# Kernel tuning notes

Hardware: AMD Instinct MI355X
Metric: run time of the kernel (lower is better)

The kernel has to match this reference:

```python
import jax, jax.numpy as jnp
import numpy as np

K = 3
KK = K * K


def _offset_mask_conv(x, ow, ob):
    # Conv2d(C_in, 3*KK, k=3, stride=1, pad=1) in NCHW/OIHW
    y = jax.lax.conv_general_dilated(
        x, ow, window_strides=(1, 1), padding=((1, 1), (1, 1)),
        dimension_numbers=('NCHW', 'OIHW', 'NCHW'))
    return y + ob[None, :, None, None]


def _bilinear(xb, gy, gx):
    # xb: [C,H,W]; gy,gx: [KK,H,W] pixel coords (align_corners=True => pixel==unnormalized)
    # padding_mode='zeros': out-of-range taps contribute 0.
    C, H, W = xb.shape
    x0f = jnp.floor(gx); y0f = jnp.floor(gy)
    x0 = x0f.astype(jnp.int32); y0 = y0f.astype(jnp.int32)
    x1 = x0 + 1; y1 = y0 + 1
    wx1 = gx - x0f; wy1 = gy - y0f
    wx0 = 1.0 - wx1; wy0 = 1.0 - wy1

    def gather(yi, xi):
        valid = (yi >= 0) & (yi < H) & (xi >= 0) & (xi < W)
        yc = jnp.clip(yi, 0, H - 1)
        xc = jnp.clip(xi, 0, W - 1)
        v = xb[:, yc, xc]  # [C,KK,H,W]
        return v * valid[None].astype(xb.dtype)

    return (gather(y0, x0) * (wy0 * wx0)[None]
            + gather(y0, x1) * (wy0 * wx1)[None]
            + gather(y1, x0) * (wy1 * wx0)[None]
            + gather(y1, x1) * (wy1 * wx1)[None])  # [C,KK,H,W]


def setup_inputs() -> dict:
    key = jax.random.key(0)
    k1, k2, k3, k4 = jax.random.split(key, 4)
    B, C, Cout, H, W = 8, 64, 64, 128, 128
    x = jax.random.normal(k1, (B, C, H, W), dtype=jnp.float32)
    # offset/mask conv params (small, so offsets stay in a realistic range)
    ow = jax.random.normal(k2, (3 * KK, C, K, K), dtype=jnp.float32) * 0.01
    ob = jnp.zeros((3 * KK,), dtype=jnp.float32)
    # main conv weight (kaiming-ish scale) and bias
    w = jax.random.normal(k3, (Cout, C, K, K), dtype=jnp.float32) * (1.0 / np.sqrt(C * KK))
    b = jax.random.normal(k4, (Cout,), dtype=jnp.float32) * 0.01
    return {"x": x, "ow": ow, "ob": ob, "w": w, "b": b}


def reference(x, ow, ob, w, b):
    B, C, H, W = x.shape
    om = _offset_mask_conv(x, ow, ob)            # [B, 3*KK, H, W]
    off_x = om[:, :KK]                           # o1 -> x-offset
    off_y = om[:, KK:2 * KK]                     # o2 -> y-offset
    mask = jax.nn.sigmoid(om[:, 2 * KK:])        # [B,KK,H,W]

    gh, gw = jnp.meshgrid(jnp.arange(H, dtype=x.dtype), jnp.arange(W, dtype=x.dtype), indexing='ij')
    d = jnp.arange(-(K // 2), K // 2 + 1, dtype=x.dtype)
    kh, kw = jnp.meshgrid(d, d, indexing='ij')
    dh = kh.reshape(-1)                          # [KK] row-major (dh,dw) order matches weight[...,i,j]
    dw = kw.reshape(-1)

    gx = gw[None, None] + dw[None, :, None, None] + off_x   # [B,KK,H,W]
    gy = gh[None, None] + dh[None, :, None, None] + off_y

    sampled = jax.vmap(_bilinear)(x, gy, gx)     # [B,C,KK,H,W]
    sampled = sampled * mask[:, None]            # modulation

    wflat = w.reshape(w.shape[0], w.shape[1], KK)  # [Cout,C,KK]
    out = jnp.einsum('bckhw,ock->bohw', sampled, wflat) + b[None, :, None, None]
    return out
```

## Files before the change

### kernel.cpp

```cpp
#include <hip/hip_runtime.h>

#define B 8
#define C 64
#define H 128
#define W 128
#define HW (H * W)
#define OC 27
#define KK 9
#define COUT 64
#define KDIM 576
#define LDSROW 1152
#define NPIX 32
#define NMETA (NPIX * KK)

typedef __attribute__((ext_vector_type(8))) short s16x8;
typedef __attribute__((ext_vector_type(4))) float f32x4;

__device__ inline ushort f2bf(float f) {
    union { float f; unsigned u; } uv;
    uv.f = f;
    unsigned r = uv.u + 0x7FFF + ((uv.u >> 16) & 1);
    return (ushort)(r >> 16);
}
__device__ inline float bf2f(ushort u) {
    return __uint_as_float((unsigned)u << 16);
}

__global__ __launch_bounds__(256) void k_transpose_x(const float* __restrict__ x,
                                                     ushort* __restrict__ xTb) {
    __shared__ float lds[64][65];
    int j = blockIdx.x;
    int vb = (j & 7) * 256 + (j >> 3);
    int b = vb >> 8;
    int tile = vb & 255;
    int hw0 = tile * 64;
    int lane = threadIdx.x & 63;
    int cg = threadIdx.x >> 6;
#pragma unroll
    for (int r = 0; r < 16; ++r) {
        int c = cg * 16 + r;
        lds[c][lane] = x[(size_t)(b * C + c) * HW + hw0 + lane];
    }
    __syncthreads();
#pragma unroll
    for (int r = 0; r < 16; ++r) {
        int hwl = cg * 16 + r;
        xTb[(size_t)(b * HW + hw0 + hwl) * C + lane] = f2bf(lds[lane][hwl]);
    }
}

__global__ __launch_bounds__(256) void k_prep_w(const float* __restrict__ w,
                                                ushort* __restrict__ wB) {
    int idx = blockIdx.x * 256 + threadIdx.x;
    if (idx >= COUT * KDIM) return;
    int o = idx / KDIM;
    int Kx = idx % KDIM;
    int k = Kx >> 6;
    int c = Kx & 63;
    wB[idx] = f2bf(w[(size_t)(o * C + c) * KK + k]);
}

__global__ __launch_bounds__(256) void k_prep_aw(const float* __restrict__ ow,
                                                 ushort* __restrict__ awB) {
    int idx = blockIdx.x * 256 + threadIdx.x;
    if (idx >= 32 * KDIM) return;
    int o = idx / KDIM;
    int Kx = idx % KDIM;
    int tap = Kx >> 6;
    int c = Kx & 63;
    float v = (o < OC) ? ow[((size_t)o * C + c) * KK + tap] : 0.0f;
    awB[idx] = f2bf(v);
}

__global__ __launch_bounds__(256) void k_om(const ushort* __restrict__ xTb,
                                            const ushort* __restrict__ awB,
                                            const float* __restrict__ ob,
                                            float* __restrict__ om_pm) {
    __shared__ __align__(16) char xwin[3 * 66 * 128];
    int tid = threadIdx.x;
    int lane = tid & 63;
    int wv = tid >> 6;
    int j = blockIdx.x;
    int vb = (j & 7) * 256 + (j >> 3);
    int b = vb >> 8;
    int h = (vb >> 1) & 127;
    int w0 = (vb & 1) * 64;

    const ushort* xb = xTb + (size_t)b * (HW * C);
    int ch2 = tid & 31;
#pragma unroll
    for (int it = 0; it < 25; ++it) {
        int pi = it * 8 + (tid >> 5);
        if (pi < 198) {
            int row = pi / 66;
            int col = pi - row * 66;
            int y = h - 1 + row;
            int xc = w0 - 1 + col;
            unsigned v = 0;
            if ((unsigned)y < H && (unsigned)xc < W)
                v = *(const unsigned*)(xb + ((size_t)(y * W + xc) << 6) + ch2 * 2);
            int byte = (pi * 128 + ch2 * 4) ^ ((col & 7) << 4);
            *(unsigned*)(xwin + byte) = v;
        }
    }
    __syncthreads();

    f32x4 acc0 = {0.f, 0.f, 0.f, 0.f};
    f32x4 acc1 = {0.f, 0.f, 0.f, 0.f};
    int pixl = lane & 15;
    int q = lane >> 4;
    int base_col = wv * 16 + pixl;
    const ushort* a0 = awB + (size_t)pixl * KDIM + q * 8;
    const ushort* a1 = awB + (size_t)(16 + pixl) * KDIM + q * 8;
#pragma unroll
    for (int s = 0; s < 18; ++s) {
        int tap = s >> 1;
        int row = tap / 3;
        int cs = tap - row * 3;
        int col = base_col + cs;
        int c0b = ((s & 1) * 32 + q * 8) * 2;
        int byte = (((row * 66 + col) << 7) + c0b) ^ ((col & 7) << 4);
        s16x8 bfrag = *(const s16x8*)(xwin + byte);
        s16x8 af0 = *(const s16x8*)(a0 + s * 32);
        s16x8 af1 = *(const s16x8*)(a1 + s * 32);
        acc0 = __builtin_amdgcn_mfma_f32_16x16x32_bf16(af0, bfrag, acc0, 0, 0, 0);
        acc1 = __builtin_amdgcn_mfma_f32_16x16x32_bf16(af1, bfrag, acc1, 0, 0, 0);
    }

    __syncthreads();
    float* omt = (float*)xwin;
    {
        int pix = wv * 16 + pixl;
#pragma unroll
        for (int jj = 0; jj < 4; ++jj) {
            int oc = q * 4 + jj;
            omt[pix * 29 + oc] = acc0[jj] + ob[oc];
        }
#pragma unroll
        for (int jj = 0; jj < 4; ++jj) {
            int oc1 = 16 + q * 4 + jj;
            if (oc1 < OC) omt[pix * 29 + oc1] = acc1[jj] + ob[oc1];
        }
    }
    __syncthreads();

    float* dst = om_pm + ((size_t)b * HW + h * W + w0) * 32;
#pragma unroll
    for (int t = tid; t < 64 * 32; t += 256) {
        int pix = t >> 5;
        int oc = t & 31;
        float v = (oc < OC) ? omt[pix * 29 + oc] : 0.0f;
        dst[(size_t)pix * 32 + oc] = v;
    }
}

__global__ __launch_bounds__(512) void k_main(const ushort* __restrict__ xTb,
                                              const float* __restrict__ om_pm,
                                              const ushort* __restrict__ wB,
                                              const float* __restrict__ bias,
                                              float* __restrict__ out) {
    __shared__ __align__(16) char smem[NPIX * LDSROW];
    __shared__ float4 mw_lds[NMETA];
    __shared__ int2 mo_lds[NMETA];

    int tid = threadIdx.x;
    int lane = tid & 63;
    int wv = tid >> 6;
    int jb = blockIdx.x;
    int vb = (jb & 7) * 512 + (jb >> 3);
    int pb = vb * NPIX;
    int b = pb >> 14;
    int rem = pb & (HW - 1);
    int h = rem >> 7;
    int w0 = rem & (W - 1);

    if (tid < NMETA) {
        int pix = tid / 9;
        int k = tid - pix * 9;
        const float* o0 = om_pm + ((size_t)b * HW + rem + pix) * 32;
        float offx = o0[k];
        float offy = o0[9 + k];
        float mlog = o0[18 + k];
        int dh = k / 3 - 1;
        int dw = k % 3 - 1;
        float mask = 1.0f / (1.0f + __expf(-mlog));
        float gx = (float)(w0 + pix + dw) + offx;
        float gy = (float)(h + dh) + offy;
        float x0f = floorf(gx), y0f = floorf(gy);
        int x0 = (int)x0f, y0 = (int)y0f;
        int x1 = x0 + 1, y1 = y0 + 1;
        float wx1 = gx - x0f, wy1 = gy - y0f;
        float wx0 = 1.0f - wx1, wy0 = 1.0f - wy1;
        float rw0 = ((unsigned)y0 < H) ? wy0 * mask : 0.0f;
        float rw1 = ((unsigned)y1 < H) ? wy1 * mask : 0.0f;
        int y0c = min(max(y0, 0), H - 1), y1c = min(max(y1, 0), H - 1);
        int colbase = min(max(x0, 0), W - 2);
        float cw0 = 0.0f, cw1 = 0.0f;
        if ((unsigned)x0 < W) { if (x0 == colbase) cw0 += wx0; else cw1 += wx0; }
        if ((unsigned)x1 < W) { if (x1 == colbase) cw0 += wx1; else cw1 += wx1; }
        mw_lds[tid] = make_float4(rw0 * cw0, rw0 * cw1, rw1 * cw0, rw1 * cw1);
        mo_lds[tid] = make_int2((y0c * W + colbase) * (C * 2),
                                (y1c * W + colbase) * (C * 2));
    }
    __syncthreads();

    const char* xbase = (const char*)(xTb + (size_t)b * (HW * C));
    bool lo_half = lane < 32;
#pragma unroll 1
    for (int pp = 0; pp < 4; ++pp) {
        int p = wv * 4 + pp;
        float4 mwv[KK];
        int2 mov[KK];
#pragma unroll
        for (int k = 0; k < KK; ++k) {
            mwv[k] = mw_lds[p * 9 + k];
            mov[k] = mo_lds[p * 9 + k];
        }
        unsigned d0[KK], d1[KK];
#pragma unroll
        for (int k = 0; k < KK; ++k) {
            d0[k] = *(const unsigned*)(xbase + mov[k].x + lane * 4);
            d1[k] = *(const unsigned*)(xbase + mov[k].y + lane * 4);
        }
        __builtin_amdgcn_sched_barrier(0);
        int vlds = p * LDSROW + (((lane & 31) * 4) ^ ((p & 7) << 4));
#pragma unroll
        for (int k = 0; k < KK; ++k) {
            float wa = lo_half ? mwv[k].x : mwv[k].y;
            float wb_ = lo_half ? mwv[k].z : mwv[k].w;
            float a0 = __uint_as_float(d0[k] << 16);
            float a1 = __uint_as_float(d0[k] & 0xFFFF0000u);
            float b0 = __uint_as_float(d1[k] << 16);
            float b1 = __uint_as_float(d1[k] & 0xFFFF0000u);
            float p0 = a0 * wa + b0 * wb_;
            float p1 = a1 * wa + b1 * wb_;
            float q0 = __shfl_xor(p0, 32, 64);
            float q1 = __shfl_xor(p1, 32, 64);
            float s0 = p0 + q0, s1 = p1 + q1;
            unsigned pk;
            asm("v_cvt_pk_bf16_f32 %0, %1, %2" : "=v"(pk) : "v"(s0), "v"(s1));
            if (lane < 32) *(unsigned*)(smem + vlds + k * 128) = pk;
        }
    }
    __syncthreads();

    int mrow = (wv & 3) * 16;
    int pixsel = ((wv >> 2) << 4) + (lane & 15);
    f32x4 acc;
#pragma unroll
    for (int j = 0; j < 4; ++j) acc[j] = bias[mrow + (lane >> 4) * 4 + j];

    const ushort* wrow = wB + (size_t)(mrow + (lane & 15)) * KDIM + (lane >> 4) * 8;
#pragma unroll
    for (int s = 0; s < 18; ++s) {
        int kbyte = s * 64 + (lane >> 4) * 16;
        int byte = (pixsel * LDSROW + kbyte) ^ ((pixsel & 7) << 4);
        s16x8 bfrag = *(const s16x8*)(smem + byte);
        s16x8 afrag = *(const s16x8*)(wrow + s * 32);
        acc = __builtin_amdgcn_mfma_f32_16x16x32_bf16(afrag, bfrag, acc, 0, 0, 0);
    }

    float* obase = out + ((size_t)(b * COUT + mrow + (lane >> 4) * 4) * HW) + h * W +
                   w0 + ((wv >> 2) << 4);
#pragma unroll
    for (int j = 0; j < 4; ++j) obase[(size_t)j * HW + (lane & 15)] = acc[j];
}

extern "C" void kernel_launch(void* const* d_in, const int* in_sizes, int n_in,
                              void* d_out, int out_size, void* d_ws, size_t ws_size,
                              hipStream_t stream) {
    const float* x = (const float*)d_in[0];
    const float* ow = (const float*)d_in[1];
    const float* ob = (const float*)d_in[2];
    const float* w = (const float*)d_in[3];
    const float* bias = (const float*)d_in[4];
    float* out = (float*)d_out;

    float* om_pm = (float*)d_ws;
    ushort* xTb = (ushort*)(om_pm + (size_t)B * HW * 32);
    ushort* wB = xTb + (size_t)B * HW * C;
    ushort* awB = wB + (size_t)COUT * KDIM;

    hipLaunchKernelGGL(k_transpose_x, dim3(B * 256), dim3(256), 0, stream, x, xTb);
    hipLaunchKernelGGL(k_prep_w, dim3((COUT * KDIM + 255) / 256), dim3(256), 0,
                       stream, w, wB);
    hipLaunchKernelGGL(k_prep_aw, dim3((32 * KDIM + 255) / 256), dim3(256), 0,
                       stream, ow, awB);
    hipLaunchKernelGGL(k_om, dim3(B * H * 2), dim3(256), 0, stream, xTb, awB, ob, om_pm);
    hipLaunchKernelGGL(k_main, dim3(B * HW / NPIX), dim3(512), 0, stream,
                       xTb, om_pm, wB, bias, out);
}
```

Measured before the change: 180.2 us.

## Shrink main-kernel tiles to 16 pixels and compress sampling metadata to fp16/ushort

Halves the pixels per block in the fused deformable-conv kernel (16 pixels, 256 threads) and gives each wave one 16-row output slice of the MFMA stage. Bilinear tap weights are stored in LDS as packed fp16 pairs, and row offsets as 16-bit indices scaled by 128 bytes, instead of float4/int2. The aim is to cut LDS footprint and register pressure so more blocks are resident at once. In exchange, the interpolation weights lose precision by passing through fp16, and there are twice as many blocks, each carrying the same per-block overhead.

```diff
diff --git a/kernel.cpp b/kernel.cpp
--- a/kernel.cpp
+++ b/kernel.cpp
@@ -1,4 +1,5 @@
 #include <hip/hip_runtime.h>
+#include <hip/hip_fp16.h>
 
 #define B 8
 #define C 64
@@ -10,8 +11,8 @@
 #define COUT 64
 #define KDIM 576
 #define LDSROW 1152
-#define NPIX 32
-#define NMETA (NPIX * KK)
+#define NPIX 16
+#define NPAIR (NPIX * KK)
 
 typedef __attribute__((ext_vector_type(8))) short s16x8;
 typedef __attribute__((ext_vector_type(4))) float f32x4;
@@ -24,6 +25,10 @@
 }
 __device__ inline float bf2f(ushort u) {
     return __uint_as_float((unsigned)u << 16);
+}
+__device__ inline unsigned pkhalf2(float a, float b) {
+    __half2 h = __floats2half2_rn(a, b);
+    return *(unsigned*)&h;
 }
 
 __global__ __launch_bounds__(256) void k_transpose_x(const float* __restrict__ x,
@@ -154,27 +159,27 @@
     }
 }
 
-__global__ __launch_bounds__(512) void k_main(const ushort* __restrict__ xTb,
+__global__ __launch_bounds__(256) void k_main(const ushort* __restrict__ xTb,
                                               const float* __restrict__ om_pm,
                                               const ushort* __restrict__ wB,
                                               const float* __restrict__ bias,
                                               float* __restrict__ out) {
     __shared__ __align__(16) char smem[NPIX * LDSROW];
-    __shared__ float4 mw_lds[NMETA];
-    __shared__ int2 mo_lds[NMETA];
+    __shared__ uint2 mw_lds[NPAIR];
+    __shared__ ushort2 mo_lds[NPAIR];
 
     int tid = threadIdx.x;
     int lane = tid & 63;
     int wv = tid >> 6;
     int jb = blockIdx.x;
-    int vb = (jb & 7) * 512 + (jb >> 3);
+    int vb = (jb & 7) * 1024 + (jb >> 3);
     int pb = vb * NPIX;
     int b = pb >> 14;
     int rem = pb & (HW - 1);
     int h = rem >> 7;
     int w0 = rem & (W - 1);
 
-    if (tid < NMETA) {
+    if (tid < NPAIR) {
         int pix = tid / 9;
         int k = tid - pix * 9;
         const float* o0 = om_pm + ((size_t)b * HW + rem + pix) * 32;
@@ -198,9 +203,10 @@
         float cw0 = 0.0f, cw1 = 0.0f;
         if ((unsigned)x0 < W) { if (x0 == colbase) cw0 += wx0; else cw1 += wx0; }
         if ((unsigned)x1 < W) { if (x1 == colbase) cw0 += wx1; else cw1 += wx1; }
-        mw_lds[tid] = make_float4(rw0 * cw0, rw0 * cw1, rw1 * cw0, rw1 * cw1);
-        mo_lds[tid] = make_int2((y0c * W + colbase) * (C * 2),
-                                (y1c * W + colbase) * (C * 2));
+        mw_lds[tid] = make_uint2(pkhalf2(rw0 * cw0, rw0 * cw1),
+                                 pkhalf2(rw1 * cw0, rw1 * cw1));
+        mo_lds[tid] = make_ushort2((ushort)(((y0c * W + colbase) * (C * 2)) >> 7),
+                                   (ushort)(((y1c * W + colbase) * (C * 2)) >> 7));
     }
     __syncthreads();
 
@@ -209,25 +215,29 @@
 #pragma unroll 1
     for (int pp = 0; pp < 4; ++pp) {
         int p = wv * 4 + pp;
-        float4 mwv[KK];
-        int2 mov[KK];
+        uint2 mwv[KK];
+        int mo0[KK], mo1[KK];
 #pragma unroll
         for (int k = 0; k < KK; ++k) {
             mwv[k] = mw_lds[p * 9 + k];
-            mov[k] = mo_lds[p * 9 + k];
+            ushort2 mo = mo_lds[p * 9 + k];
+            mo0[k] = (int)mo.x << 7;
+            mo1[k] = (int)mo.y << 7;
         }
         unsigned d0[KK], d1[KK];
 #pragma unroll
         for (int k = 0; k < KK; ++k) {
-            d0[k] = *(const unsigned*)(xbase + mov[k].x + lane * 4);
-            d1[k] = *(const unsigned*)(xbase + mov[k].y + lane * 4);
+            d0[k] = *(const unsigned*)(xbase + mo0[k] + lane * 4);
+            d1[k] = *(const unsigned*)(xbase + mo1[k] + lane * 4);
         }
         __builtin_amdgcn_sched_barrier(0);
         int vlds = p * LDSROW + (((lane & 31) * 4) ^ ((p & 7) << 4));
 #pragma unroll
         for (int k = 0; k < KK; ++k) {
-            float wa = lo_half ? mwv[k].x : mwv[k].y;
-            float wb_ = lo_half ? mwv[k].z : mwv[k].w;
+            __half2 h0 = *(__half2*)&mwv[k].x;
+            __half2 h1 = *(__half2*)&mwv[k].y;
+            float wa = lo_half ? __half2float(h0.x) : __half2float(h0.y);
+            float wb_ = lo_half ? __half2float(h1.x) : __half2float(h1.y);
             float a0 = __uint_as_float(d0[k] << 16);
             float a1 = __uint_as_float(d0[k] & 0xFFFF0000u);
             float b0 = __uint_as_float(d1[k] << 16);
@@ -244,26 +254,24 @@
     }
     __syncthreads();
 
-    int mrow = (wv & 3) * 16;
-    int pixsel = ((wv >> 2) << 4) + (lane & 15);
     f32x4 acc;
 #pragma unroll
-    for (int j = 0; j < 4; ++j) acc[j] = bias[mrow + (lane >> 4) * 4 + j];
-
-    const ushort* wrow = wB + (size_t)(mrow + (lane & 15)) * KDIM + (lane >> 4) * 8;
+    for (int j = 0; j < 4; ++j) acc[j] = bias[wv * 16 + (lane >> 4) * 4 + j];
+
+    int pix = lane & 15;
+    const ushort* wrow = wB + (size_t)(wv * 16 + pix) * KDIM + (lane >> 4) * 8;
 #pragma unroll
     for (int s = 0; s < 18; ++s) {
         int kbyte = s * 64 + (lane >> 4) * 16;
-        int byte = (pixsel * LDSROW + kbyte) ^ ((pixsel & 7) << 4);
+        int byte = (pix * LDSROW + kbyte) ^ ((pix & 7) << 4);
         s16x8 bfrag = *(const s16x8*)(smem + byte);
         s16x8 afrag = *(const s16x8*)(wrow + s * 32);
         acc = __builtin_amdgcn_mfma_f32_16x16x32_bf16(afrag, bfrag, acc, 0, 0, 0);
     }
 
-    float* obase = out + ((size_t)(b * COUT + mrow + (lane >> 4) * 4) * HW) + h * W +
-                   w0 + ((wv >> 2) << 4);
-#pragma unroll
-    for (int j = 0; j < 4; ++j) obase[(size_t)j * HW + (lane & 15)] = acc[j];
+    float* obase = out + ((size_t)(b * COUT + wv * 16 + (lane >> 4) * 4) * HW) + h * W + w0;
+#pragma unroll
+    for (int j = 0; j < 4; ++j) obase[(size_t)j * HW + pix] = acc[j];
 }
 
 extern "C" void kernel_launch(void* const* d_in, const int* in_sizes, int n_in,
@@ -287,6 +295,6 @@
     hipLaunchKernelGGL(k_prep_aw, dim3((32 * KDIM + 255) / 256), dim3(256), 0,
                        stream, ow, awB);
     hipLaunchKernelGGL(k_om, dim3(B * H * 2), dim3(256), 0, stream, xTb, awB, ob, om_pm);
-    hipLaunchKernelGGL(k_main, dim3(B * HW / NPIX), dim3(512), 0, stream,
+    hipLaunchKernelGGL(k_main, dim3(B * HW / NPIX), dim3(256), 0, stream,
                        xTb, om_pm, wB, bias, out);
 }
```

After: 162.5 us. 9.8% less time.
